# Performance work log

Measured on AMD Instinct MI355X. Metric: run time of the kernel, lower is better.

The kernel has to match this reference:

```python
import jax, jax.numpy as jnp
import numpy as np

GROUP_SIZE = 64
M, K, N, RANK = 4096, 4096, 4096, 32


def setup_inputs() -> dict:
    key = jax.random.key(0)
    ks = jax.random.split(key, 7)
    x = jax.random.normal(ks[0], (M, K), dtype=jnp.float32)
    # int4 weight residual in [-8, 7]
    q_w = jax.random.randint(ks[1], (K, N), -8, 8, dtype=jnp.int32)
    # positive per-group weight scales, shape (K // group_size, N)
    wscales = jax.random.uniform(ks[2], (K // GROUP_SIZE, N), dtype=jnp.float32) * 0.01 + 1e-4
    lora_down = jax.random.normal(ks[3], (K, RANK), dtype=jnp.float32) * 0.02
    lora_up = jax.random.normal(ks[4], (RANK, N), dtype=jnp.float32) * 0.02
    # smoothing factors, strictly positive
    smooth = jax.random.uniform(ks[5], (K,), dtype=jnp.float32) + 0.5
    bias = jax.random.normal(ks[6], (N,), dtype=jnp.float32)
    return {"x": x, "q_w": q_w, "wscales": wscales, "lora_down": lora_down,
            "lora_up": lora_up, "smooth": smooth, "bias": bias}


def reference(x, q_w, wscales, lora_down, lora_up, smooth, bias):
    G = GROUP_SIZE
    m, k = x.shape
    n = q_w.shape[1]
    ng = k // G  # groups along K

    # smooth activation: move outliers into weights
    x_smooth = x / smooth[None, :]

    # per-group symmetric int4 quantize + dequantize of activations
    xg = x_smooth.reshape(m, ng, G)
    ascales = jnp.maximum(jnp.max(jnp.abs(xg), axis=-1) / 7.0, 1e-8)  # (m, ng)
    qx = jnp.clip(jnp.round(xg / ascales[..., None]), -8.0, 7.0)
    x_dq = (qx * ascales[..., None]).reshape(m, k)

    # dequantize int4 weight residual: grouped along K
    W_dq = (q_w.astype(jnp.float32).reshape(ng, G, n) * wscales[:, None, :]).reshape(k, n)

    # simulated int4 GEMM + fp LoRA residual + bias
    y_main = x_dq @ W_dq
    y_lora = (x @ lora_down) @ lora_up
    return y_main + y_lora + bias[None, :]
```

## Files before the change

### kernel.cpp

```cpp
#include <hip/hip_runtime.h>
#include <hip/hip_bf16.h>
#include <stdint.h>

#define GSIZE 64
#define MDIM 4096
#define KDIM 4096
#define NDIM 4096
#define RANK 32
#define KE   4160
#define NG   64
#define NSPLIT 8

#define N_LORAT (32 * NSPLIT)
#define B_WPREP0 N_LORAT
#define N_WPREP (65 * 64)
#define B_QUANT0 (B_WPREP0 + N_WPREP)
#define NBLOCKS  (B_QUANT0 + MDIM)

typedef __bf16 bf16x4 __attribute__((ext_vector_type(4)));
typedef __bf16 bf16x8 __attribute__((ext_vector_type(8)));
typedef float  f32x4  __attribute__((ext_vector_type(4)));

#define GPTR(p) ((__attribute__((address_space(1))) void*)(uintptr_t)(p))
#define LPTR(p) ((__attribute__((address_space(3))) void*)(p))

__global__ __launch_bounds__(256) void k_prep(const float* __restrict__ x,
                                              const int*   __restrict__ qw,
                                              const float* __restrict__ wsc,
                                              const float* __restrict__ ld,
                                              const float* __restrict__ lu,
                                              const float* __restrict__ smooth,
                                              __bf16* __restrict__ A,
                                              __bf16* __restrict__ Wt,
                                              float* __restrict__ tws) {
    __shared__ __attribute__((aligned(16))) char smem[10240];
    int b   = blockIdx.x;
    int tid = threadIdx.x;

    if (b < N_LORAT) {
        __bf16* AsL = (__bf16*)smem;
        __bf16* BsL = (__bf16*)(smem + 8192);
        int m0    = (b & 31) * 128;
        int sp    = b >> 5;
        int kbase = sp * 512;
        int lane = tid & 63;
        int wave = tid >> 6;
        int quad = lane >> 4;
        int mrow = lane & 15;

        f32x4 z = {0.f, 0.f, 0.f, 0.f};
        f32x4 acc[2][2];
        acc[0][0] = z; acc[0][1] = z; acc[1][0] = z; acc[1][1] = z;

        for (int step = 0; step < 16; ++step) {
            int kk = kbase + step * 32;
            #pragma unroll
            for (int it = 0; it < 2; ++it) {
                int slot = it * 256 + tid;
                int r = slot >> 2;
                int g = (slot & 3) ^ (r & 3);
                const float* src = x + (size_t)(m0 + r) * KDIM + kk + g * 8;
                float4 a0 = *(const float4*)src;
                float4 a1 = *(const float4*)(src + 4);
                bf16x8 v = {(__bf16)a0.x, (__bf16)a0.y, (__bf16)a0.z, (__bf16)a0.w,
                            (__bf16)a1.x, (__bf16)a1.y, (__bf16)a1.z, (__bf16)a1.w};
                *(bf16x8*)(AsL + slot * 8) = v;
            }
            #pragma unroll
            for (int i2 = 0; i2 < 4; ++i2) {
                int j = i2 * 256 + tid;
                int r = j >> 5, n = j & 31;
                BsL[n * 32 + r] = (__bf16)ld[(size_t)(kk + r) * RANK + n];
            }
            __syncthreads();
            bf16x8 av[2], bv[2];
            #pragma unroll
            for (int i = 0; i < 2; ++i) {
                int row  = wave * 32 + i * 16 + mrow;
                int slot = row * 4 + (quad ^ (row & 3));
                av[i] = *(const bf16x8*)(AsL + slot * 8);
            }
            #pragma unroll
            for (int j = 0; j < 2; ++j)
                bv[j] = *(const bf16x8*)(BsL + (j * 16 + mrow) * 32 + quad * 8);
            #pragma unroll
            for (int i = 0; i < 2; ++i)
                #pragma unroll
                for (int j = 0; j < 2; ++j)
                    acc[i][j] = __builtin_amdgcn_mfma_f32_16x16x32_bf16(av[i], bv[j], acc[i][j], 0, 0, 0);
            __syncthreads();
        }
        float* tout = tws + (size_t)sp * MDIM * RANK;
        #pragma unroll
        for (int i = 0; i < 2; ++i)
            #pragma unroll
            for (int j = 0; j < 2; ++j)
                #pragma unroll
                for (int r = 0; r < 4; ++r) {
                    int rowg = m0 + wave * 32 + i * 16 + quad * 4 + r;
                    int col  = j * 16 + mrow;
                    tout[(size_t)rowg * RANK + col] = acc[i][j][r];
                }
        return;
    }

    if (b < B_QUANT0) {
        __bf16 (*tile)[68] = (__bf16(*)[68])smem;
        int idx = b - B_WPREP0;
        int n0 = (idx & 63) * 64;
        int kt = idx >> 6;
        int k0 = kt * 64;
        int tr = tid >> 4;
        int tc = (tid & 15) * 4;
        if (kt < NG) {
            float4 ws = *(const float4*)(wsc + (size_t)kt * NDIM + n0 + tc);
            #pragma unroll
            for (int r = tr; r < 64; r += 16) {
                int4 q = *(const int4*)(qw + (size_t)(k0 + r) * NDIM + n0 + tc);
                tile[r][tc + 0] = (__bf16)((float)q.x * ws.x);
                tile[r][tc + 1] = (__bf16)((float)q.y * ws.y);
                tile[r][tc + 2] = (__bf16)((float)q.z * ws.z);
                tile[r][tc + 3] = (__bf16)((float)q.w * ws.w);
            }
        } else {
            #pragma unroll
            for (int r = tr; r < 64; r += 16) {
                if (r < RANK) {
                    float4 lv = *(const float4*)(lu + (size_t)r * NDIM + n0 + tc);
                    tile[r][tc + 0] = (__bf16)lv.x;
                    tile[r][tc + 1] = (__bf16)lv.y;
                    tile[r][tc + 2] = (__bf16)lv.z;
                    tile[r][tc + 3] = (__bf16)lv.w;
                } else {
                    tile[r][tc + 0] = (__bf16)0.f;
                    tile[r][tc + 1] = (__bf16)0.f;
                    tile[r][tc + 2] = (__bf16)0.f;
                    tile[r][tc + 3] = (__bf16)0.f;
                }
            }
        }
        __syncthreads();
        int nn = tid >> 3;
        int ks = (tid & 7) * 8;
        #pragma unroll
        for (int p = 0; p < 2; ++p) {
            int n = nn + p * 32;
            bf16x8 v;
            #pragma unroll
            for (int e = 0; e < 8; ++e) v[e] = tile[ks + e][n];
            *(bf16x8*)(Wt + (size_t)(n0 + n) * KE + k0 + ks) = v;
        }
        return;
    }

    {
        int row = b - B_QUANT0;
        const float4* xr4 = (const float4*)(x + (size_t)row * KDIM);
        const float4* sm4 = (const float4*)smooth;
        __bf16* ar = A + (size_t)row * KE;
        #pragma unroll
        for (int p = 0; p < 4; ++p) {
            int i4 = p * 256 + tid;
            float4 xv = xr4[i4];
            float4 sv = sm4[i4];
            float4 xs = {xv.x * __builtin_amdgcn_rcpf(sv.x),
                         xv.y * __builtin_amdgcn_rcpf(sv.y),
                         xv.z * __builtin_amdgcn_rcpf(sv.z),
                         xv.w * __builtin_amdgcn_rcpf(sv.w)};
            float a = fmaxf(fmaxf(fabsf(xs.x), fabsf(xs.y)),
                            fmaxf(fabsf(xs.z), fabsf(xs.w)));
            #pragma unroll
            for (int off = 1; off < 16; off <<= 1)
                a = fmaxf(a, __shfl_xor(a, off, 64));
            float ascale = fmaxf(a * (1.0f / 7.0f), 1e-8f);
            float rin = __builtin_amdgcn_rcpf(ascale);
            float q0 = fminf(fmaxf(rintf(xs.x * rin), -8.f), 7.f);
            float q1 = fminf(fmaxf(rintf(xs.y * rin), -8.f), 7.f);
            float q2 = fminf(fmaxf(rintf(xs.z * rin), -8.f), 7.f);
            float q3 = fminf(fmaxf(rintf(xs.w * rin), -8.f), 7.f);
            bf16x4 av = {(__bf16)(q0 * ascale), (__bf16)(q1 * ascale),
                         (__bf16)(q2 * ascale), (__bf16)(q3 * ascale)};
            *(bf16x4*)(ar + i4 * 4) = av;
        }
    }
}

__global__ __launch_bounds__(256) void k_fin(const float* __restrict__ tws,
                                             __bf16* __restrict__ A) {
    int idx = blockIdx.x * 256 + threadIdx.x;
    int m = idx >> 4, cq = idx & 15;
    int c = cq * 4;
    bf16x4 v = {(__bf16)0.f, (__bf16)0.f, (__bf16)0.f, (__bf16)0.f};
    if (c < RANK) {
        f32x4 s = {0.f, 0.f, 0.f, 0.f};
        #pragma unroll
        for (int sp = 0; sp < NSPLIT; ++sp) {
            f32x4 p = *(const f32x4*)(tws + ((size_t)sp * MDIM + m) * RANK + c);
            s.x += p.x; s.y += p.y; s.z += p.z; s.w += p.w;
        }
        v[0] = (__bf16)s.x; v[1] = (__bf16)s.y; v[2] = (__bf16)s.z; v[3] = (__bf16)s.w;
    }
    *(bf16x4*)(A + (size_t)m * KE + KDIM + c) = v;
}

#define NT (KE / 64)
#define HS 8192
#define BS 16384

#define STAGE(ldsbase, gb, kt, half) do {                                     \
    int _k0 = (kt) * 64;                                                      \
    _Pragma("unroll")                                                         \
    for (int _it = 0; _it < 2; ++_it) {                                       \
        int _c = _it * 512 + tid;                                             \
        int _r = _c >> 3;                                                     \
        int _g = (_c & 7) ^ (_r & 7);                                         \
        __builtin_amdgcn_global_load_lds(                                     \
            GPTR((gb) + (size_t)((half) * 128 + _r) * KE + _k0 + _g * 8),     \
            LPTR((char*)(ldsbase) + (_it * 512 + wave * 64) * 16),            \
            16, 0, 0);                                                        \
    } } while (0)

#define RD_A(dst, qm) do {                                                    \
    _Pragma("unroll")                                                         \
    for (int _i = 0; _i < 4; ++_i) {                                          \
        int _row = (qm) * 128 + wm * 64 + _i * 16 + mrow;                     \
        dst[0][_i] = *(const bf16x8*)((const char*)Acur + _row * 128 + ga0 * 16); \
        dst[1][_i] = *(const bf16x8*)((const char*)Acur + _row * 128 + ga1 * 16); \
    } } while (0)

#define RD_B(dst, qn) do {                                                    \
    _Pragma("unroll")                                                         \
    for (int _j = 0; _j < 2; ++_j) {                                          \
        int _row = (qn) * 128 + wn * 32 + _j * 16 + mrow;                     \
        dst[0][_j] = *(const bf16x8*)((const char*)Bcur + _row * 128 + ga0 * 16); \
        dst[1][_j] = *(const bf16x8*)((const char*)Bcur + _row * 128 + ga1 * 16); \
    } } while (0)

#define MMA(qm, qn, AV, BV) do {                                              \
    _Pragma("unroll")                                                         \
    for (int _i = 0; _i < 4; ++_i)                                            \
        _Pragma("unroll")                                                     \
        for (int _j = 0; _j < 2; ++_j) {                                      \
            acc[qm][qn][_i][_j] = __builtin_amdgcn_mfma_f32_16x16x32_bf16(    \
                AV[0][_i], BV[0][_j], acc[qm][qn][_i][_j], 0, 0, 0);          \
            acc[qm][qn][_i][_j] = __builtin_amdgcn_mfma_f32_16x16x32_bf16(    \
                AV[1][_i], BV[1][_j], acc[qm][qn][_i][_j], 0, 0, 0);          \
        } } while (0)

#define PH_SYNC() do {                                                        \
    __builtin_amdgcn_s_barrier();                                             \
    asm volatile("s_waitcnt lgkmcnt(0)" ::: "memory");                        \
    __builtin_amdgcn_sched_barrier(0); } while (0)

__global__ __launch_bounds__(512, 2) void k_gemm(const __bf16* __restrict__ A,
                                                 const __bf16* __restrict__ Wt,
                                                 const float*  __restrict__ bias,
                                                 float* __restrict__ out) {
    __shared__ __attribute__((aligned(16))) __bf16 As[2 * BS];
    __shared__ __attribute__((aligned(16))) __bf16 Bs[2 * BS];
    int tid  = threadIdx.x;
    int lane = tid & 63;
    int wave = tid >> 6;
    int quad = lane >> 4;
    int mrow = lane & 15;
    int wm = wave >> 2;
    int wn = wave & 3;
    int m0 = blockIdx.y * 256, n0 = blockIdx.x * 256;

    const __bf16* Ab = A  + (size_t)m0 * KE;
    const __bf16* Bb = Wt + (size_t)n0 * KE;

    int ga0 = quad ^ (mrow & 7);
    int ga1 = (quad + 4) ^ (mrow & 7);

    f32x4 z = {0.f, 0.f, 0.f, 0.f};
    f32x4 acc[2][2][4][2];
    #pragma unroll
    for (int a = 0; a < 2; ++a)
        #pragma unroll
        for (int b = 0; b < 2; ++b)
            #pragma unroll
            for (int i = 0; i < 4; ++i)
                #pragma unroll
                for (int j = 0; j < 2; ++j) acc[a][b][i][j] = z;

    STAGE(As,           Ab, 0, 0);
    STAGE(Bs + HS,      Bb, 0, 1);
    STAGE(Bs,           Bb, 0, 0);
    STAGE(As + HS,      Ab, 0, 1);
    STAGE(As + BS,      Ab, 1, 0);
    STAGE(Bs + BS + HS, Bb, 1, 1);
    asm volatile("s_waitcnt vmcnt(4)" ::: "memory");
    __builtin_amdgcn_s_barrier();

    for (int t = 0; t < NT; ++t) {
        int cur = t & 1;
        const __bf16* Acur = As + cur * BS;
        const __bf16* Bcur = Bs + cur * BS;
        __bf16* Anx = As + (cur ^ 1) * BS;
        __bf16* Bnx = Bs + (cur ^ 1) * BS;
        __bf16* Acu = As + cur * BS;
        __bf16* Bcu = Bs + cur * BS;
        bool s1 = (t + 1 < NT), s2 = (t + 2 < NT);

        bf16x8 av0[2][4], av1[2][4], bv0[2][2], bv1[2][2];

        RD_A(av0, 0);
        RD_B(bv0, 0);
        if (s1) STAGE(Bnx, Bb, t + 1, 0);
        PH_SYNC();
        __builtin_amdgcn_s_setprio(1);
        MMA(0, 0, av0, bv0);
        __builtin_amdgcn_s_setprio(0);
        __builtin_amdgcn_s_barrier();

        RD_B(bv1, 1);
        if (s1) STAGE(Anx + HS, Ab, t + 1, 1);
        PH_SYNC();
        __builtin_amdgcn_s_setprio(1);
        MMA(0, 1, av0, bv1);
        __builtin_amdgcn_s_setprio(0);
        __builtin_amdgcn_s_barrier();

        RD_A(av1, 1);
        if (s2) STAGE(Acu, Ab, t + 2, 0);
        PH_SYNC();
        __builtin_amdgcn_s_setprio(1);
        MMA(1, 1, av1, bv1);
        __builtin_amdgcn_s_setprio(0);
        __builtin_amdgcn_s_barrier();

        if (s2) STAGE(Bcu + HS, Bb, t + 2, 1);
        __builtin_amdgcn_s_barrier();
        __builtin_amdgcn_s_setprio(1);
        MMA(1, 0, av1, bv0);
        __builtin_amdgcn_s_setprio(0);
        if (s2) { asm volatile("s_waitcnt vmcnt(4)" ::: "memory"); }
        else    { asm volatile("s_waitcnt vmcnt(0)" ::: "memory"); }
        __builtin_amdgcn_s_barrier();
    }

    #pragma unroll
    for (int qn = 0; qn < 2; ++qn)
        #pragma unroll
        for (int j = 0; j < 2; ++j) {
            int col = n0 + qn * 128 + wn * 32 + j * 16 + mrow;
            float bvs = bias[col];
            #pragma unroll
            for (int qm = 0; qm < 2; ++qm)
                #pragma unroll
                for (int i = 0; i < 4; ++i) {
                    int rbase = m0 + qm * 128 + wm * 64 + i * 16 + quad * 4;
                    #pragma unroll
                    for (int r = 0; r < 4; ++r)
                        __builtin_nontemporal_store(acc[qm][qn][i][j][r] + bvs,
                                                    &out[(size_t)(rbase + r) * NDIM + col]);
                }
        }
}

extern "C" void kernel_launch(void* const* d_in, const int* in_sizes, int n_in,
                              void* d_out, int out_size, void* d_ws, size_t ws_size,
                              hipStream_t stream) {
    const float* x    = (const float*)d_in[0];
    const int*   qw   = (const int*)  d_in[1];
    const float* wsc  = (const float*)d_in[2];
    const float* ld   = (const float*)d_in[3];
    const float* lu   = (const float*)d_in[4];
    const float* sm   = (const float*)d_in[5];
    const float* bias = (const float*)d_in[6];
    float* out = (float*)d_out;

    char* ws = (char*)d_ws;
    __bf16* A   = (__bf16*)ws;
    __bf16* Wt  = (__bf16*)(ws + (size_t)MDIM * KE * 2);
    float*  tws = (float*) (ws + (size_t)MDIM * KE * 4);

    k_prep<<<NBLOCKS, 256, 0, stream>>>(x, qw, wsc, ld, lu, sm, A, Wt, tws);
    k_fin<<<(MDIM * 16) / 256, 256, 0, stream>>>(tws, A);
    k_gemm<<<dim3(NDIM / 256, MDIM / 256), 512, 0, stream>>>(A, Wt, bias, out);
}
```

Before: 321.6 us.

## Software-pipeline LDS fragment reads ahead of MFMA phases in GEMM loop

Restructures the main GEMM loop so LDS-to-register fragment reads for the next phase, and the next K tile's first A/B fragments, are issued before the current MFMA block runs. Full barrier+lgkmcnt(0) syncs are replaced with partial lgkmcnt waits and sched_barriers, and several workgroup barriers are dropped. The aim is to hide LDS read latency behind matrix math and cut barrier stalls. In exchange it raises register pressure, and the tightened vmcnt/barrier placement risks races if the wait counts do not match the outstanding loads.

```diff
diff --git a/kernel.cpp b/kernel.cpp
--- a/kernel.cpp
+++ b/kernel.cpp
@@ -220,20 +220,20 @@
             16, 0, 0);                                                        \
     } } while (0)
 
-#define RD_A(dst, qm) do {                                                    \
+#define RD_A(dst, base, qm) do {                                              \
     _Pragma("unroll")                                                         \
     for (int _i = 0; _i < 4; ++_i) {                                          \
         int _row = (qm) * 128 + wm * 64 + _i * 16 + mrow;                     \
-        dst[0][_i] = *(const bf16x8*)((const char*)Acur + _row * 128 + ga0 * 16); \
-        dst[1][_i] = *(const bf16x8*)((const char*)Acur + _row * 128 + ga1 * 16); \
+        dst[0][_i] = *(const bf16x8*)((const char*)(base) + _row * 128 + ga0 * 16); \
+        dst[1][_i] = *(const bf16x8*)((const char*)(base) + _row * 128 + ga1 * 16); \
     } } while (0)
 
-#define RD_B(dst, qn) do {                                                    \
+#define RD_B(dst, base, qn) do {                                              \
     _Pragma("unroll")                                                         \
     for (int _j = 0; _j < 2; ++_j) {                                          \
         int _row = (qn) * 128 + wn * 32 + _j * 16 + mrow;                     \
-        dst[0][_j] = *(const bf16x8*)((const char*)Bcur + _row * 128 + ga0 * 16); \
-        dst[1][_j] = *(const bf16x8*)((const char*)Bcur + _row * 128 + ga1 * 16); \
+        dst[0][_j] = *(const bf16x8*)((const char*)(base) + _row * 128 + ga0 * 16); \
+        dst[1][_j] = *(const bf16x8*)((const char*)(base) + _row * 128 + ga1 * 16); \
     } } while (0)
 
 #define MMA(qm, qn, AV, BV) do {                                              \
@@ -247,10 +247,7 @@
                 AV[1][_i], BV[1][_j], acc[qm][qn][_i][_j], 0, 0, 0);          \
         } } while (0)
 
-#define PH_SYNC() do {                                                        \
-    __builtin_amdgcn_s_barrier();                                             \
-    asm volatile("s_waitcnt lgkmcnt(0)" ::: "memory");                        \
-    __builtin_amdgcn_sched_barrier(0); } while (0)
+#define SBAR0() __builtin_amdgcn_sched_barrier(0)
 
 __global__ __launch_bounds__(512, 2) void k_gemm(const __bf16* __restrict__ A,
                                                  const __bf16* __restrict__ Wt,
@@ -292,6 +289,12 @@
     STAGE(Bs + BS + HS, Bb, 1, 1);
     asm volatile("s_waitcnt vmcnt(4)" ::: "memory");
     __builtin_amdgcn_s_barrier();
+    SBAR0();
+
+    bf16x8 av0[2][4], av1[2][4], bv0[2][2], bv1[2][2];
+    RD_A(av0, As, 0);
+    RD_B(bv0, Bs, 0);
+    SBAR0();
 
     for (int t = 0; t < NT; ++t) {
         int cur = t & 1;
@@ -303,41 +306,46 @@
         __bf16* Bcu = Bs + cur * BS;
         bool s1 = (t + 1 < NT), s2 = (t + 2 < NT);
 
-        bf16x8 av0[2][4], av1[2][4], bv0[2][2], bv1[2][2];
-
-        RD_A(av0, 0);
-        RD_B(bv0, 0);
         if (s1) STAGE(Bnx, Bb, t + 1, 0);
-        PH_SYNC();
+        RD_B(bv1, Bcur, 1);
+        SBAR0();
+        asm volatile("s_waitcnt lgkmcnt(4)" ::: "memory");
+        SBAR0();
         __builtin_amdgcn_s_setprio(1);
         MMA(0, 0, av0, bv0);
         __builtin_amdgcn_s_setprio(0);
-        __builtin_amdgcn_s_barrier();
-
-        RD_B(bv1, 1);
+
         if (s1) STAGE(Anx + HS, Ab, t + 1, 1);
-        PH_SYNC();
+        RD_A(av1, Acur, 1);
+        SBAR0();
+        asm volatile("s_waitcnt lgkmcnt(8)" ::: "memory");
+        SBAR0();
         __builtin_amdgcn_s_setprio(1);
         MMA(0, 1, av0, bv1);
         __builtin_amdgcn_s_setprio(0);
         __builtin_amdgcn_s_barrier();
-
-        RD_A(av1, 1);
+        SBAR0();
+
         if (s2) STAGE(Acu, Ab, t + 2, 0);
-        PH_SYNC();
+        SBAR0();
+        asm volatile("s_waitcnt lgkmcnt(0)" ::: "memory");
+        SBAR0();
         __builtin_amdgcn_s_setprio(1);
         MMA(1, 1, av1, bv1);
         __builtin_amdgcn_s_setprio(0);
+        if (s2) { asm volatile("s_waitcnt vmcnt(2)" ::: "memory"); }
+        else    { asm volatile("s_waitcnt vmcnt(0)" ::: "memory"); }
         __builtin_amdgcn_s_barrier();
+        SBAR0();
 
         if (s2) STAGE(Bcu + HS, Bb, t + 2, 1);
-        __builtin_amdgcn_s_barrier();
+        if (s1) RD_A(av0, Anx, 0);
+        SBAR0();
         __builtin_amdgcn_s_setprio(1);
         MMA(1, 0, av1, bv0);
         __builtin_amdgcn_s_setprio(0);
-        if (s2) { asm volatile("s_waitcnt vmcnt(4)" ::: "memory"); }
-        else    { asm volatile("s_waitcnt vmcnt(0)" ::: "memory"); }
-        __builtin_amdgcn_s_barrier();
+        if (s1) RD_B(bv0, Bnx, 0);
+        SBAR0();
     }
 
     #pragma unroll
```

Result: no change. 320.5 us (-0.4%).
